# Kernel tuning notes

Hardware: AMD Instinct MI355X
Metric: run time of the kernel (lower is better)

The kernel has to match this reference:

```python
import jax, jax.numpy as jnp
import numpy as np

EPS = 1e-12  # F.normalize eps
CLAMP = 30.0
POS_W = 1.0
NEG_W = 1.0
LABEL_SMOOTHING = 0.0


def _l2_normalize(x):
    n = jnp.sqrt(jnp.sum(x * x, axis=-1, keepdims=True))
    return x / jnp.maximum(n, EPS)


def setup_inputs() -> dict:
    key = jax.random.key(0)
    kv, kt = jax.random.split(key)
    B, D = 8192, 512
    video_features = jax.random.normal(kv, (B, D), dtype=jnp.float32)
    text_features = jax.random.normal(kt, (B, D), dtype=jnp.float32)
    log_temp = jnp.asarray(np.log(0.07), dtype=jnp.float32)  # typical CLIP init
    bias = jnp.asarray(-10.0, dtype=jnp.float32)  # bias_init
    return {
        "video_features": video_features,
        "text_features": text_features,
        "log_temp": log_temp,
        "bias": bias,
    }


def reference(video_features, text_features, log_temp, bias):
    v = _l2_normalize(video_features.astype(jnp.float32))  # [B_v, D]
    t = _l2_normalize(text_features.astype(jnp.float32))   # [B_t, D]
    sim = jnp.einsum("vd,td->vt", v, t)                    # [B_v, B_t]
    temp = jnp.exp(log_temp.astype(jnp.float32))
    logits = jnp.clip(sim / temp + bias, -CLAMP, CLAMP)
    B_v, B_t = v.shape[0], t.shape[0]
    m = min(B_v, B_t)
    # diagonal positive labels (pos_mask is None path)
    labels = jnp.zeros((B_v, B_t), jnp.float32).at[jnp.arange(m), jnp.arange(m)].set(1.0)
    if LABEL_SMOOTHING > 0:
        labels = labels * (1 - LABEL_SMOOTHING) + LABEL_SMOOTHING / 2
    weights = jnp.where(labels > 0.5, POS_W, NEG_W).astype(jnp.float32)
    # numerically stable BCE-with-logits, elementwise then weighted mean
    z = logits
    bce = jnp.maximum(z, 0.0) - z * labels + jnp.log1p(jnp.exp(-jnp.abs(z)))
    return jnp.mean(weights * bce)
```

## Files before the change

kernel.cpp:

```cpp
#include <hip/hip_runtime.h>
#include <cstdint>

#define NB 8192
#define ND 512
#define BM 256
#define BN 256
#define BK 64
#define NT (ND / BK)
#define THREADS 512

typedef __bf16 bf16x8 __attribute__((ext_vector_type(8)));
typedef float f32x4 __attribute__((ext_vector_type(4)));

__device__ __forceinline__ unsigned short f2bf(float f) {
    union { float f; uint32_t u; } c; c.f = f;
    return (unsigned short)((c.u + 0x7fffu + ((c.u >> 16) & 1u)) >> 16);
}

__device__ __forceinline__ void load16(const void* g, void* l) {
    __builtin_amdgcn_global_load_lds(
        (void __attribute__((address_space(1)))*)(const_cast<void*>(g)),
        (void __attribute__((address_space(3)))*)(l),
        16, 0, 0);
}

__global__ __launch_bounds__(256) void norm_cast(const float* __restrict__ v,
                                                 const float* __restrict__ t,
                                                 unsigned short* __restrict__ vn,
                                                 unsigned short* __restrict__ tn,
                                                 int ns) {
    const int wave = threadIdx.x >> 6;
    const int lane = threadIdx.x & 63;
    const int row = blockIdx.x * 4 + wave;
    const float* src;
    unsigned short* dst;
    if (row < NB) { src = v + (size_t)row * ND; dst = vn + (size_t)row * ns; }
    else { src = t + (size_t)(row - NB) * ND; dst = tn + (size_t)(row - NB) * ns; }
    float4 a = ((const float4*)src)[lane * 2];
    float4 b = ((const float4*)src)[lane * 2 + 1];
    float ss = a.x * a.x + a.y * a.y + a.z * a.z + a.w * a.w
             + b.x * b.x + b.y * b.y + b.z * b.z + b.w * b.w;
#pragma unroll
    for (int off = 32; off; off >>= 1) ss += __shfl_xor(ss, off);
    const float sc = 1.0f / fmaxf(sqrtf(ss), 1e-12f);
    union { unsigned short us[8]; uint4 q; } pk;
    pk.us[0] = f2bf(a.x * sc); pk.us[1] = f2bf(a.y * sc);
    pk.us[2] = f2bf(a.z * sc); pk.us[3] = f2bf(a.w * sc);
    pk.us[4] = f2bf(b.x * sc); pk.us[5] = f2bf(b.y * sc);
    pk.us[6] = f2bf(b.z * sc); pk.us[7] = f2bf(b.w * sc);
    ((uint4*)dst)[lane] = pk.q;
}

__global__ __launch_bounds__(THREADS, 2) void gemm_bce(const unsigned short* __restrict__ vn,
                                                       const unsigned short* __restrict__ tn,
                                                       const float* __restrict__ lt,
                                                       const float* __restrict__ bp,
                                                       float* __restrict__ out_sum,
                                                       int ns) {
    __shared__ __align__(16) unsigned short smem[2 * 2 * BM * BK];
    __shared__ float red[8];

    const int tid = threadIdx.x;
    const int lane = tid & 63;
    const int wave = tid >> 6;
    const int wr = wave >> 2;
    const int wc = wave & 3;
    const int lq = lane & 15;
    const int lh = lane >> 4;

    const int m0 = (int)(blockIdx.x >> 5) * BM;
    const int n0 = (int)(blockIdx.x & 31) * BN;

    const int sr = tid >> 3;
    const int sc = (tid & 7) ^ (sr & 7);
    const unsigned short* sA = vn + (size_t)(m0 + sr) * ns + sc * 8;
    const unsigned short* sB = tn + (size_t)(n0 + sr) * ns + sc * 8;

#define STG_A(B, T, H) do {                                                    \
        unsigned short* _d = smem + (B) * 32768 + (((H) * 128) + wave * 8) * 64; \
        load16(sA + (size_t)((H) * 128) * ns + (T) * 64, _d);                  \
        load16(sA + (size_t)((H) * 128 + 64) * ns + (T) * 64, _d + 4096);      \
    } while (0)
#define STG_B(B, T, H) do {                                                    \
        unsigned short* _d = smem + (B) * 32768 + 16384 + (((H) * 128) + wave * 8) * 64; \
        load16(sB + (size_t)((H) * 128) * ns + (T) * 64, _d);                  \
        load16(sB + (size_t)((H) * 128 + 64) * ns + (T) * 64, _d + 4096);      \
    } while (0)

    const int s0 = ((lh ^ (lq & 7)) * 8);
    const int aro = (wr * 16 + lq) * 64;
    const int bro = (wc * 16 + lq) * 64;
#define RD_A(C, M, KS) (*(const bf16x8*)(smem + (C) * 32768 + aro + (M) * 2048 + ((KS) ? (s0 ^ 32) : s0)))
#define RD_B(C, N, KS) (*(const bf16x8*)(smem + (C) * 32768 + 16384 + bro + (N) * 4096 + ((KS) ? (s0 ^ 32) : s0)))

#define BAR __builtin_amdgcn_s_barrier()
#define SCB __builtin_amdgcn_sched_barrier(0)
#define LGK0 asm volatile("s_waitcnt lgkmcnt(0)" ::: "memory")
#define VM12 asm volatile("s_waitcnt vmcnt(12)" ::: "memory")
#define VM10 asm volatile("s_waitcnt vmcnt(10)" ::: "memory")
#define VM8  asm volatile("s_waitcnt vmcnt(8)" ::: "memory")
#define VM6  asm volatile("s_waitcnt vmcnt(6)" ::: "memory")
#define VM2  asm volatile("s_waitcnt vmcnt(2)" ::: "memory")
#define VM0  asm volatile("s_waitcnt vmcnt(0)" ::: "memory")
#define VMNONE ((void)0)

    f32x4 acc[8][4];
#pragma unroll
    for (int m = 0; m < 8; ++m)
#pragma unroll
        for (int n = 0; n < 4; ++n)
            acc[m][n] = f32x4{0.f, 0.f, 0.f, 0.f};

    bf16x8 afr[4][2], bfr[4][2];

#define MFMA16(MB, N0)                                                          \
    _Pragma("unroll") for (int mm = 0; mm < 4; ++mm)                            \
    _Pragma("unroll") for (int nn = 0; nn < 2; ++nn)                            \
    _Pragma("unroll") for (int kk = 0; kk < 2; ++kk)                            \
        acc[(MB) + mm][(N0) + nn] = __builtin_amdgcn_mfma_f32_16x16x32_bf16(    \
            afr[mm][kk], bfr[(N0) + nn][kk], acc[(MB) + mm][(N0) + nn], 0, 0, 0)

#define TILE_BODY(T, S123, S4, W1, W2, W4) do {                                 \
                                               \
        _Pragma("unroll") for (int mm = 0; mm < 4; ++mm) {                      \
            afr[mm][0] = RD_A((T) & 1, mm, 0); afr[mm][1] = RD_A((T) & 1, mm, 1); } \
        _Pragma("unroll") for (int nn = 0; nn < 2; ++nn) {                      \
            bfr[nn][0] = RD_B((T) & 1, nn, 0); bfr[nn][1] = RD_B((T) & 1, nn, 1); } \
        if (S123) STG_B(((T) & 1) ^ 1, (T) + 1, 0);                             \
        BAR; LGK0; SCB;                                                         \
        __builtin_amdgcn_s_setprio(1); MFMA16(0, 0);                            \
        __builtin_amdgcn_s_setprio(0); W1; BAR; SCB;                            \
                                                         \
        _Pragma("unroll") for (int nn = 2; nn < 4; ++nn) {                      \
            bfr[nn][0] = RD_B((T) & 1, nn, 0); bfr[nn][1] = RD_B((T) & 1, nn, 1); } \
        if (S123) STG_B(((T) & 1) ^ 1, (T) + 1, 1);                             \
        BAR; LGK0; SCB;                                                         \
        __builtin_amdgcn_s_setprio(1); MFMA16(0, 2);                            \
        __builtin_amdgcn_s_setprio(0); W2; BAR; SCB;                            \
                                      \
        _Pragma("unroll") for (int mm = 0; mm < 4; ++mm) {                      \
            afr[mm][0] = RD_A((T) & 1, mm + 4, 0); afr[mm][1] = RD_A((T) & 1, mm + 4, 1); } \
        if (S123) STG_A(((T) & 1) ^ 1, (T) + 1, 1);                             \
        BAR; LGK0; SCB;                                                         \
        __builtin_amdgcn_s_setprio(1); MFMA16(4, 0);                            \
        __builtin_amdgcn_s_setprio(0); BAR; SCB;                                \
                                                \
        if (S4) STG_A((T) & 1, (T) + 2, 0);                                     \
        BAR; SCB;                                                               \
        __builtin_amdgcn_s_setprio(1); MFMA16(4, 2);                            \
        __builtin_amdgcn_s_setprio(0); W4; BAR; SCB;                            \
    } while (0)

    STG_A(0, 0, 0); STG_B(0, 0, 0); STG_B(0, 0, 1); STG_A(0, 0, 1);
    STG_A(1, 1, 0); STG_B(1, 1, 0); STG_B(1, 1, 1); STG_A(1, 1, 1);
    VM12; BAR; SCB;

    TILE_BODY(0, false, true,  VM10, VM8, VM6);
    TILE_BODY(1, true,  true,  VM6,  VM6, VM6);
    TILE_BODY(2, true,  true,  VM6,  VM6, VM6);
    TILE_BODY(3, true,  true,  VM6,  VM6, VM6);
    TILE_BODY(4, true,  true,  VM6,  VM6, VM6);
    TILE_BODY(5, true,  true,  VM6,  VM6, VM6);
    TILE_BODY(6, true,  false, VM6,  VM6, VM6);
    TILE_BODY(7, false, false, VM2,  VM0, VMNONE);

    const float invtemp = __expf(-lt[0]);
    const float bias = bp[0];
    float local = 0.f;
    const int row_base = m0 + wr * 16 + lh * 4;
    const int col_base = n0 + wc * 16 + lq;
#pragma unroll
    for (int m = 0; m < 8; ++m) {
#pragma unroll
        for (int n = 0; n < 4; ++n) {
#pragma unroll
            for (int r = 0; r < 4; ++r) {
                const float s = acc[m][n][r];
                float z = fminf(fmaxf(fmaf(s, invtemp, bias), -30.f), 30.f);
                const int gr = row_base + m * 32 + r;
                const int gc = col_base + n * 64;
                local += fmaxf(z, 0.f) + __logf(1.0f + __expf(-fabsf(z))) - ((gr == gc) ? z : 0.f);
            }
        }
    }
#pragma unroll
    for (int off = 32; off; off >>= 1) local += __shfl_xor(local, off);
    if (lane == 0) red[wave] = local;
    __syncthreads();
    if (tid == 0) {
        float tot = 0.f;
#pragma unroll
        for (int w = 0; w < 8; ++w) tot += red[w];
        atomicAdd(out_sum, tot * (1.0f / 67108864.0f));
    }
}

extern "C" void kernel_launch(void* const* d_in, const int* in_sizes, int n_in,
                              void* d_out, int out_size, void* d_ws, size_t ws_size,
                              hipStream_t stream) {
    const float* v = (const float*)d_in[0];
    const float* t = (const float*)d_in[1];
    const float* lt = (const float*)d_in[2];
    const float* bp = (const float*)d_in[3];
    float* out = (float*)d_out;

    const size_t need = (size_t)2 * NB * ND * sizeof(unsigned short);
    unsigned short *vn, *tn;
    int ns;
    if (ws_size >= need) {
        vn = (unsigned short*)d_ws;
        tn = vn + (size_t)NB * ND;
        ns = ND;
    } else {
        vn = (unsigned short*)d_in[0];
        tn = (unsigned short*)d_in[1];
        ns = ND * 2;
    }

    hipMemsetAsync(out, 0, sizeof(float), stream);
    hipLaunchKernelGGL(norm_cast, dim3((2 * NB) / 4), dim3(256), 0, stream, v, t, vn, tn, ns);
    hipLaunchKernelGGL(gemm_bce, dim3((NB / BM) * (NB / BN)), dim3(THREADS), 0, stream,
                       vn, tn, lt, bp, out, ns);
}
```

Measured before the change: 176.5 us.

## Switch GEMM mainloop to BK=32 triple-buffered LDS pipeline with one barrier per tile

Halves the K tile to 32 and uses three LDS buffers instead of two. Each tile issues its global-to-LDS loads two tiles ahead and synchronises with a single vmcnt wait and barrier, replacing the four barrier-separated phases per BK=64 tile. The LDS swizzle and read offsets are redone for the 32-wide rows. This cuts barrier count and tries to hide load latency better, at the cost of twice as many K iterations. LDS use drops from 64 KB to 48 KB per block.

New measurement: 176.3 us. About the same (-0.1%).

```diff
diff --git a/kernel.cpp b/kernel.cpp
--- a/kernel.cpp
+++ b/kernel.cpp
@@ -5,9 +5,10 @@
 #define ND 512
 #define BM 256
 #define BN 256
-#define BK 64
-#define NT (ND / BK)
+#define BK 32
+#define NTL (ND / BK)
 #define THREADS 512
+#define BUFS 16384
 
 typedef __bf16 bf16x8 __attribute__((ext_vector_type(8)));
 typedef float f32x4 __attribute__((ext_vector_type(4)));
@@ -57,7 +58,7 @@
                                                        const float* __restrict__ bp,
                                                        float* __restrict__ out_sum,
                                                        int ns) {
-    __shared__ __align__(16) unsigned short smem[2 * 2 * BM * BK];
+    __shared__ __align__(16) unsigned short smem[3 * BUFS];
     __shared__ float red[8];
 
     const int tid = threadIdx.x;
@@ -71,38 +72,29 @@
     const int m0 = (int)(blockIdx.x >> 5) * BM;
     const int n0 = (int)(blockIdx.x & 31) * BN;
 
-    const int sr = tid >> 3;
-    const int sc = (tid & 7) ^ (sr & 7);
-    const unsigned short* sA = vn + (size_t)(m0 + sr) * ns + sc * 8;
-    const unsigned short* sB = tn + (size_t)(n0 + sr) * ns + sc * 8;
+    const int schunk = ((lane & 3) ^ ((lane >> 3) & 3)) * 8;
+    const unsigned short* sA = vn + (size_t)(m0 + 32 * wave + (lane >> 2)) * ns + schunk;
+    const unsigned short* sB = tn + (size_t)(n0 + 32 * wave + (lane >> 2)) * ns + schunk;
 
-#define STG_A(B, T, H) do {                                                    \
-        unsigned short* _d = smem + (B) * 32768 + (((H) * 128) + wave * 8) * 64; \
-        load16(sA + (size_t)((H) * 128) * ns + (T) * 64, _d);                  \
-        load16(sA + (size_t)((H) * 128 + 64) * ns + (T) * 64, _d + 4096);      \
-    } while (0)
-#define STG_B(B, T, H) do {                                                    \
-        unsigned short* _d = smem + (B) * 32768 + 16384 + (((H) * 128) + wave * 8) * 64; \
-        load16(sB + (size_t)((H) * 128) * ns + (T) * 64, _d);                  \
-        load16(sB + (size_t)((H) * 128 + 64) * ns + (T) * 64, _d + 4096);      \
+#define STG(T, B) do {                                                         \
+        unsigned short* _dA = smem + (B) * BUFS + wave * 1024;                 \
+        unsigned short* _dB = _dA + 8192;                                      \
+        load16(sA + (T) * 32, _dA);                                            \
+        load16(sA + (T) * 32 + (size_t)16 * ns, _dA + 512);                    \
+        load16(sB + (T) * 32, _dB);                                            \
+        load16(sB + (T) * 32 + (size_t)16 * ns, _dB + 512);                    \
     } while (0)
 
-    const int s0 = ((lh ^ (lq & 7)) * 8);
-    const int aro = (wr * 16 + lq) * 64;
-    const int bro = (wc * 16 + lq) * 64;
-#define RD_A(C, M, KS) (*(const bf16x8*)(smem + (C) * 32768 + aro + (M) * 2048 + ((KS) ? (s0 ^ 32) : s0)))
-#define RD_B(C, N, KS) (*(const bf16x8*)(smem + (C) * 32768 + 16384 + bro + (N) * 4096 + ((KS) ? (s0 ^ 32) : s0)))
+    const int sl = (lh ^ ((lq >> 1) & 3)) * 8;
+    const int aro = (wr * 16 + lq) * 32 + sl;
+    const int bro = (wc * 16 + lq) * 32 + sl;
+#define RD_A(C, M) (*(const bf16x8*)(smem + (C) * BUFS + aro + (M) * 1024))
+#define RD_B(C, N) (*(const bf16x8*)(smem + (C) * BUFS + 8192 + bro + (N) * 2048))
 
 #define BAR __builtin_amdgcn_s_barrier()
 #define SCB __builtin_amdgcn_sched_barrier(0)
-#define LGK0 asm volatile("s_waitcnt lgkmcnt(0)" ::: "memory")
-#define VM12 asm volatile("s_waitcnt vmcnt(12)" ::: "memory")
-#define VM10 asm volatile("s_waitcnt vmcnt(10)" ::: "memory")
-#define VM8  asm volatile("s_waitcnt vmcnt(8)" ::: "memory")
-#define VM6  asm volatile("s_waitcnt vmcnt(6)" ::: "memory")
-#define VM2  asm volatile("s_waitcnt vmcnt(2)" ::: "memory")
-#define VM0  asm volatile("s_waitcnt vmcnt(0)" ::: "memory")
-#define VMNONE ((void)0)
+#define VM4 asm volatile("s_waitcnt vmcnt(4)" ::: "memory")
+#define VM0 asm volatile("s_waitcnt vmcnt(0)" ::: "memory")
 
     f32x4 acc[8][4];
 #pragma unroll
@@ -111,58 +103,41 @@
         for (int n = 0; n < 4; ++n)
             acc[m][n] = f32x4{0.f, 0.f, 0.f, 0.f};
 
-    bf16x8 afr[4][2], bfr[4][2];
+    bf16x8 afr[8], bfr[4];
 
-#define MFMA16(MB, N0)                                                          \
-    _Pragma("unroll") for (int mm = 0; mm < 4; ++mm)                            \
-    _Pragma("unroll") for (int nn = 0; nn < 2; ++nn)                            \
-    _Pragma("unroll") for (int kk = 0; kk < 2; ++kk)                            \
-        acc[(MB) + mm][(N0) + nn] = __builtin_amdgcn_mfma_f32_16x16x32_bf16(    \
-            afr[mm][kk], bfr[(N0) + nn][kk], acc[(MB) + mm][(N0) + nn], 0, 0, 0)
-
-#define TILE_BODY(T, S123, S4, W1, W2, W4) do {                                 \
-                                               \
-        _Pragma("unroll") for (int mm = 0; mm < 4; ++mm) {                      \
-            afr[mm][0] = RD_A((T) & 1, mm, 0); afr[mm][1] = RD_A((T) & 1, mm, 1); } \
-        _Pragma("unroll") for (int nn = 0; nn < 2; ++nn) {                      \
-            bfr[nn][0] = RD_B((T) & 1, nn, 0); bfr[nn][1] = RD_B((T) & 1, nn, 1); } \
-        if (S123) STG_B(((T) & 1) ^ 1, (T) + 1, 0);                             \
-        BAR; LGK0; SCB;                                                         \
-        __builtin_amdgcn_s_setprio(1); MFMA16(0, 0);                            \
-        __builtin_amdgcn_s_setprio(0); W1; BAR; SCB;                            \
-                                                         \
-        _Pragma("unroll") for (int nn = 2; nn < 4; ++nn) {                      \
-            bfr[nn][0] = RD_B((T) & 1, nn, 0); bfr[nn][1] = RD_B((T) & 1, nn, 1); } \
-        if (S123) STG_B(((T) & 1) ^ 1, (T) + 1, 1);                             \
-        BAR; LGK0; SCB;                                                         \
-        __builtin_amdgcn_s_setprio(1); MFMA16(0, 2);                            \
-        __builtin_amdgcn_s_setprio(0); W2; BAR; SCB;                            \
-                                      \
-        _Pragma("unroll") for (int mm = 0; mm < 4; ++mm) {                      \
-            afr[mm][0] = RD_A((T) & 1, mm + 4, 0); afr[mm][1] = RD_A((T) & 1, mm + 4, 1); } \
-        if (S123) STG_A(((T) & 1) ^ 1, (T) + 1, 1);                             \
-        BAR; LGK0; SCB;                                                         \
-        __builtin_amdgcn_s_setprio(1); MFMA16(4, 0);                            \
-        __builtin_amdgcn_s_setprio(0); BAR; SCB;                                \
-                                                \
-        if (S4) STG_A((T) & 1, (T) + 2, 0);                                     \
-        BAR; SCB;                                                               \
-        __builtin_amdgcn_s_setprio(1); MFMA16(4, 2);                            \
-        __builtin_amdgcn_s_setprio(0); W4; BAR; SCB;                            \
+#define TILE(T, S, WMODE) do {                                                  \
+                                       \
+        _Pragma("unroll") for (int mm = 0; mm < 4; ++mm) afr[mm] = RD_A((T) % 3, mm); \
+        _Pragma("unroll") for (int nn = 0; nn < 4; ++nn) bfr[nn] = RD_B((T) % 3, nn); \
+        SCB;                                                                    \
+           \
+        _Pragma("unroll") for (int mm = 4; mm < 8; ++mm) afr[mm] = RD_A((T) % 3, mm); \
+        if (S) STG((T) + 2, ((T) + 2) % 3);                                     \
+        SCB;                                                                    \
+        __builtin_amdgcn_s_setprio(1);                                          \
+        _Pragma("unroll") for (int mm = 0; mm < 4; ++mm)                        \
+        _Pragma("unroll") for (int nn = 0; nn < 4; ++nn)                        \
+            acc[mm][nn] = __builtin_amdgcn_mfma_f32_16x16x32_bf16(              \
+                afr[mm], bfr[nn], acc[mm][nn], 0, 0, 0);                        \
+        __builtin_amdgcn_s_setprio(0); SCB;                                     \
+        __builtin_amdgcn_s_setprio(1);                                          \
+        _Pragma("unroll") for (int mm = 4; mm < 8; ++mm)                        \
+        _Pragma("unroll") for (int nn = 0; nn < 4; ++nn)                        \
+            acc[mm][nn] = __builtin_amdgcn_mfma_f32_16x16x32_bf16(              \
+                afr[mm], bfr[nn], acc[mm][nn], 0, 0, 0);                        \
+        __builtin_amdgcn_s_setprio(0); SCB;                                     \
+        if ((WMODE) == 0) { VM4; BAR; SCB; }                                    \
+        else if ((WMODE) == 1) { VM0; BAR; SCB; }                               \
     } while (0)
 
-    STG_A(0, 0, 0); STG_B(0, 0, 0); STG_B(0, 0, 1); STG_A(0, 0, 1);
-    STG_A(1, 1, 0); STG_B(1, 1, 0); STG_B(1, 1, 1); STG_A(1, 1, 1);
-    VM12; BAR; SCB;
+    STG(0, 0);
+    STG(1, 1);
+    VM4; BAR; SCB;
 
-    TILE_BODY(0, false, true,  VM10, VM8, VM6);
-    TILE_BODY(1, true,  true,  VM6,  VM6, VM6);
-    TILE_BODY(2, true,  true,  VM6,  VM6, VM6);
-    TILE_BODY(3, true,  true,  VM6,  VM6, VM6);
-    TILE_BODY(4, true,  true,  VM6,  VM6, VM6);
-    TILE_BODY(5, true,  true,  VM6,  VM6, VM6);
-    TILE_BODY(6, true,  false, VM6,  VM6, VM6);
-    TILE_BODY(7, false, false, VM2,  VM0, VMNONE);
+    TILE(0,  true, 0);  TILE(1,  true, 0);  TILE(2,  true, 0);  TILE(3,  true, 0);
+    TILE(4,  true, 0);  TILE(5,  true, 0);  TILE(6,  true, 0);  TILE(7,  true, 0);
+    TILE(8,  true, 0);  TILE(9,  true, 0);  TILE(10, true, 0);  TILE(11, true, 0);
+    TILE(12, true, 0);  TILE(13, true, 0);  TILE(14, false, 1); TILE(15, false, 2);
 
     const float invtemp = __expf(-lt[0]);
     const float bias = bp[0];
```
